# Kernel tuning notes

Hardware: AMD Instinct MI355X
Metric: run time of the kernel (lower is better)

The kernel has to match this reference:

```python
import jax, jax.numpy as jnp
import numpy as np

B, S, D, H = 4, 1024, 1024, 16
DEPTH = D // H


def setup_inputs() -> dict:
    key = jax.random.key(0)
    ks = jax.random.split(key, 12)
    scale = 1.0 / np.sqrt(D)
    return {
        "query": jax.random.normal(ks[0], (B, S, D), jnp.float32),
        "key_in": jax.random.normal(ks[1], (B, S, D), jnp.float32),
        "value": jax.random.normal(ks[2], (B, S, D), jnp.float32),
        "mask": jnp.zeros((B, 1, 1, S), jnp.float32),
        "wq": jax.random.normal(ks[3], (D, D), jnp.float32) * scale,
        "bq": jnp.zeros((D,), jnp.float32),
        "wk": jax.random.normal(ks[4], (D, D), jnp.float32) * scale,
        "bk": jnp.zeros((D,), jnp.float32),
        "wv": jax.random.normal(ks[5], (D, D), jnp.float32) * scale,
        "bv": jnp.zeros((D,), jnp.float32),
        "wo": jax.random.normal(ks[6], (D, D), jnp.float32) * scale,
        "bo": jnp.zeros((D,), jnp.float32),
    }


def _split_heads(x):
    b, s, _ = x.shape
    return x.reshape(b, s, H, DEPTH).transpose(0, 2, 1, 3)  # [B,H,S,depth]


def reference(query, key_in, value, mask, wq, bq, wk, bk, wv, bv, wo, bo):
    q = _split_heads(query @ wq + bq)
    k = _split_heads(key_in @ wk + bk)
    v = _split_heads(value @ wv + bv)
    # scaled dot-product attention, full O(S^2) scores as in the original
    scores = jnp.einsum("bhqd,bhkd->bhqk", q, k) / jnp.sqrt(jnp.float32(DEPTH))
    scores = scores + mask * (-1e9)
    attn = jax.nn.softmax(scores, axis=-1)
    ctx = jnp.einsum("bhqk,bhkd->bhqd", attn, v)
    concat = ctx.transpose(0, 2, 1, 3).reshape(query.shape[0], -1, D)
    return concat @ wo + bo
```

## Files before the change

### kernel.cpp

```cpp
#include <hip/hip_runtime.h>
#include <hip/hip_bf16.h>
#include <stdint.h>

#define B_ 4
#define S_ 1024
#define D_ 1024
#define H_ 16
#define DEPTH_ 64

typedef __attribute__((ext_vector_type(8))) short bf16x8;
typedef __attribute__((ext_vector_type(4))) float f32x4;
typedef unsigned short ubf16;

#define BAR() do { asm volatile("" ::: "memory"); __builtin_amdgcn_s_barrier(); asm volatile("" ::: "memory"); } while (0)

__device__ __forceinline__ ubf16 f2bf(float f) {
  union { float f; unsigned u; } v; v.f = f;
  unsigned r = v.u + 0x7fffu + ((v.u >> 16) & 1u);
  return (ubf16)(r >> 16);
}

__device__ __forceinline__ void async16(void* lds, const void* g) {
  __builtin_amdgcn_global_load_lds(
      (const __attribute__((address_space(1))) void*)g,
      (__attribute__((address_space(3))) void*)lds, 16, 0, 0);
}

struct Tp4 { const float* W[4]; ubf16* WT[4]; };
__global__ __launch_bounds__(256) void transpose4_bf16(Tp4 a) {
  __shared__ float tile[32][33];
  const float* W = a.W[blockIdx.z];
  ubf16* WT = a.WT[blockIdx.z];
  int n0 = blockIdx.x * 32, k0 = blockIdx.y * 32;
  int tx = threadIdx.x & 31, ty = threadIdx.x >> 5;
#pragma unroll
  for (int i = 0; i < 4; ++i)
    tile[ty + i * 8][tx] = W[(size_t)(k0 + ty + i * 8) * D_ + n0 + tx];
  __syncthreads();
#pragma unroll
  for (int i = 0; i < 4; ++i)
    WT[(size_t)(n0 + ty + i * 8) * D_ + k0 + tx] = f2bf(tile[tx][ty + i * 8]);
}

struct GemmUnitF {
  const float* A; const ubf16* BT; const float* bias; void* out; int mode;
};
struct GemmArgsF { GemmUnitF u[3]; };

__global__ __launch_bounds__(256) void gemm_qkv_fused(GemmArgsF args) {
  const GemmUnitF gu = args.u[blockIdx.z];
  const int orig = blockIdx.x + (blockIdx.y << 3);
  const int xcd = orig & 7, j = orig >> 3;
  const int bm0 = (xcd * 4 + (j & 3)) * 128;
  const int bn0 = (j >> 2) * 128;
  const int tid = threadIdx.x, wid = tid >> 6, lane = tid & 63;
  const int wr = wid >> 1, wc = wid & 1;
  const int l15 = lane & 15, l4 = lane >> 4;
  const int K = 1024;

  __shared__ __align__(16) ubf16 As[2][128 * 32];
  __shared__ __align__(16) ubf16 Bs[2][128 * 32];
  f32x4 acc[4][4] = {};

  int cc0, cc1;
  const float* aP0; const float* aP1;
  const ubf16* bP0; const ubf16* bP1;
  {
    cc0 = tid;           int r0 = cc0 >> 2, s0 = cc0 & 3, g0 = s0 ^ ((r0 >> 1) & 3);
    cc1 = 256 + tid;     int r1 = cc1 >> 2, s1 = cc1 & 3, g1 = s1 ^ ((r1 >> 1) & 3);
    aP0 = gu.A + (size_t)(bm0 + r0) * K + g0 * 8;
    aP1 = gu.A + (size_t)(bm0 + r1) * K + g1 * 8;
    bP0 = gu.BT + (size_t)(bn0 + r0) * K + g0 * 8;
    bP1 = gu.BT + (size_t)(bn0 + r1) * K + g1 * 8;
  }
  int aOff[4], bOff[4];
#pragma unroll
  for (int f = 0; f < 4; ++f) {
    int ra = wr * 64 + f * 16 + l15;
    aOff[f] = ra * 64 + (l4 ^ ((ra >> 1) & 3)) * 16;
    int rb = wc * 64 + f * 16 + l15;
    bOff[f] = rb * 64 + (l4 ^ ((rb >> 1) & 3)) * 16;
  }

  {
    f32x4 a00 = *(const f32x4*)aP0, a01 = *(const f32x4*)(aP0 + 4); aP0 += 32;
    f32x4 a10 = *(const f32x4*)aP1, a11 = *(const f32x4*)(aP1 + 4); aP1 += 32;
    async16((char*)&Bs[0][0] + wid * 1024, bP0); bP0 += 32;
    async16((char*)&Bs[0][0] + 4096 + wid * 1024, bP1); bP1 += 32;
    bf16x8 w0, w1;
#pragma unroll
    for (int q = 0; q < 4; ++q) {
      w0[q] = (short)f2bf(a00[q]); w0[4 + q] = (short)f2bf(a01[q]);
      w1[q] = (short)f2bf(a10[q]); w1[4 + q] = (short)f2bf(a11[q]);
    }
    *(bf16x8*)((char*)&As[0][0] + cc0 * 16) = w0;
    *(bf16x8*)((char*)&As[0][0] + cc1 * 16) = w1;
    asm volatile("s_waitcnt lgkmcnt(0)" ::: "memory");
  }

#pragma unroll 1
  for (int t = 0; t < 31; ++t) {
    const int cur = t & 1;
    f32x4 a00 = *(const f32x4*)aP0, a01 = *(const f32x4*)(aP0 + 4); aP0 += 32;
    f32x4 a10 = *(const f32x4*)aP1, a11 = *(const f32x4*)(aP1 + 4); aP1 += 32;
    async16((char*)&Bs[cur ^ 1][0] + wid * 1024, bP0); bP0 += 32;
    async16((char*)&Bs[cur ^ 1][0] + 4096 + wid * 1024, bP1); bP1 += 32;
    __builtin_amdgcn_sched_barrier(0);
    asm volatile("s_waitcnt vmcnt(4)" ::: "memory");
    __builtin_amdgcn_s_barrier();
    __builtin_amdgcn_sched_barrier(0);
    bf16x8 af[4], bfr[4];
#pragma unroll
    for (int mi = 0; mi < 4; ++mi)
      af[mi] = *(const bf16x8*)((const char*)&As[cur][0] + aOff[mi]);
#pragma unroll
    for (int ni = 0; ni < 4; ++ni)
      bfr[ni] = *(const bf16x8*)((const char*)&Bs[cur][0] + bOff[ni]);
#pragma unroll
    for (int mi = 0; mi < 4; ++mi)
#pragma unroll
      for (int ni = 0; ni < 4; ++ni)
        acc[mi][ni] = __builtin_amdgcn_mfma_f32_16x16x32_bf16(af[mi], bfr[ni], acc[mi][ni], 0, 0, 0);
    __builtin_amdgcn_sched_barrier(0);
    bf16x8 w0, w1;
#pragma unroll
    for (int q = 0; q < 4; ++q) {
      w0[q] = (short)f2bf(a00[q]); w0[4 + q] = (short)f2bf(a01[q]);
      w1[q] = (short)f2bf(a10[q]); w1[4 + q] = (short)f2bf(a11[q]);
    }
    *(bf16x8*)((char*)&As[cur ^ 1][0] + cc0 * 16) = w0;
    *(bf16x8*)((char*)&As[cur ^ 1][0] + cc1 * 16) = w1;
    asm volatile("s_waitcnt lgkmcnt(0)" ::: "memory");
    __builtin_amdgcn_s_barrier();
  }
  asm volatile("s_waitcnt vmcnt(0)" ::: "memory");
  __builtin_amdgcn_s_barrier();
  {
    bf16x8 af[4], bfr[4];
#pragma unroll
    for (int mi = 0; mi < 4; ++mi)
      af[mi] = *(const bf16x8*)((const char*)&As[1][0] + aOff[mi]);
#pragma unroll
    for (int ni = 0; ni < 4; ++ni)
      bfr[ni] = *(const bf16x8*)((const char*)&Bs[1][0] + bOff[ni]);
#pragma unroll
    for (int mi = 0; mi < 4; ++mi)
#pragma unroll
      for (int ni = 0; ni < 4; ++ni)
        acc[mi][ni] = __builtin_amdgcn_mfma_f32_16x16x32_bf16(af[mi], bfr[ni], acc[mi][ni], 0, 0, 0);
  }

  float bv[4];
#pragma unroll
  for (int ni = 0; ni < 4; ++ni) bv[ni] = gu.bias[bn0 + wc * 64 + ni * 16 + l15];
#pragma unroll
  for (int mi = 0; mi < 4; ++mi) {
#pragma unroll
    for (int ni = 0; ni < 4; ++ni) {
#pragma unroll
      for (int r = 0; r < 4; ++r) {
        int m = bm0 + wr * 64 + mi * 16 + l4 * 4 + r;
        int n = bn0 + wc * 64 + ni * 16 + l15;
        float v = acc[mi][ni][r] + bv[ni];
        if (gu.mode == 0) {
          ((ubf16*)gu.out)[(size_t)m * 1024 + n] = f2bf(v);
        } else {
          int b = m >> 10, s = m & 1023, h = n >> 6, d = n & 63;
          ((ubf16*)gu.out)[(((size_t)(b * H_ + h)) * DEPTH_ + d) * S_ + s] = f2bf(v);
        }
      }
    }
  }
}

struct GemmUnit {
  const ubf16* A; const ubf16* BT; const float* bias; void* out; int mode;
};
struct GemmArgs { GemmUnit u[3]; };

__global__ __launch_bounds__(256) void gemm_bt(GemmArgs args, int M, int N) {
  const GemmUnit gu = args.u[blockIdx.z];
  const int orig = blockIdx.x + (blockIdx.y << 3);
  const int xcd = orig & 7, j = orig >> 3;
  const int bm0 = (xcd * 4 + (j & 3)) * 128;
  const int bn0 = (j >> 2) * 128;
  const int tid = threadIdx.x, wid = tid >> 6, lane = tid & 63;
  const int wr = wid >> 1, wc = wid & 1;
  const int l15 = lane & 15, l4 = lane >> 4;
  const int K = 1024;

  __shared__ __align__(16) ubf16 As[2][128 * 32];
  __shared__ __align__(16) ubf16 Bs[2][128 * 32];
  f32x4 acc[4][4] = {};

  const ubf16* aCur[2]; const ubf16* bCur[2];
#pragma unroll
  for (int i = 0; i < 2; ++i) {
    int c = i * 256 + tid;
    int r = c >> 2, s = c & 3;
    int cg = s ^ ((r >> 1) & 3);
    aCur[i] = gu.A + (size_t)(bm0 + r) * K + cg * 8;
    bCur[i] = gu.BT + (size_t)(bn0 + r) * K + cg * 8;
  }
  auto stageAdv = [&](int bf) {
#pragma unroll
    for (int i = 0; i < 2; ++i) {
      async16((char*)&As[bf][0] + i * 4096 + wid * 1024, aCur[i]);
      async16((char*)&Bs[bf][0] + i * 4096 + wid * 1024, bCur[i]);
      aCur[i] += 32; bCur[i] += 32;
    }
  };
  int aOff[4], bOff[4];
#pragma unroll
  for (int f = 0; f < 4; ++f) {
    int ra = wr * 64 + f * 16 + l15;
    aOff[f] = ra * 64 + (l4 ^ ((ra >> 1) & 3)) * 16;
    int rb = wc * 64 + f * 16 + l15;
    bOff[f] = rb * 64 + (l4 ^ ((rb >> 1) & 3)) * 16;
  }

  stageAdv(0);
  for (int t = 0; t < 32; ++t) {
    const int cur = t & 1;
    if (t < 31) {
      stageAdv(cur ^ 1);
      asm volatile("s_waitcnt vmcnt(4)" ::: "memory");
    } else {
      asm volatile("s_waitcnt vmcnt(0)" ::: "memory");
    }
    BAR();
    bf16x8 af[4], bfr[4];
#pragma unroll
    for (int mi = 0; mi < 4; ++mi)
      af[mi] = *(const bf16x8*)((const char*)&As[cur][0] + aOff[mi]);
#pragma unroll
    for (int ni = 0; ni < 4; ++ni)
      bfr[ni] = *(const bf16x8*)((const char*)&Bs[cur][0] + bOff[ni]);
#pragma unroll
    for (int mi = 0; mi < 4; ++mi)
#pragma unroll
      for (int ni = 0; ni < 4; ++ni)
        acc[mi][ni] = __builtin_amdgcn_mfma_f32_16x16x32_bf16(af[mi], bfr[ni], acc[mi][ni], 0, 0, 0);
    BAR();
  }

  float bv[4];
#pragma unroll
  for (int ni = 0; ni < 4; ++ni) bv[ni] = gu.bias[bn0 + wc * 64 + ni * 16 + l15];
#pragma unroll
  for (int mi = 0; mi < 4; ++mi) {
#pragma unroll
    for (int ni = 0; ni < 4; ++ni) {
#pragma unroll
      for (int r = 0; r < 4; ++r) {
        int m = bm0 + wr * 64 + mi * 16 + l4 * 4 + r;
        int n = bn0 + wc * 64 + ni * 16 + l15;
        float v = acc[mi][ni][r] + bv[ni];
        if (gu.mode == 0) {
          ((ubf16*)gu.out)[(size_t)m * N + n] = f2bf(v);
        } else if (gu.mode == 1) {
          int b = m >> 10, s = m & 1023, h = n >> 6, d = n & 63;
          ((ubf16*)gu.out)[(((size_t)(b * H_ + h)) * DEPTH_ + d) * S_ + s] = f2bf(v);
        } else {
          ((float*)gu.out)[(size_t)m * N + n] = v;
        }
      }
    }
  }
}

__global__ __launch_bounds__(512) void attention_fwd(
    const ubf16* __restrict__ Q, const ubf16* __restrict__ Kg,
    const ubf16* __restrict__ VT, const float* __restrict__ mask,
    ubf16* __restrict__ ctx) {
  const int lid = blockIdx.y * 4 + blockIdx.x;
  const int t0 = (lid & 7) * 32 + (lid >> 3);
  const int qt = t0 & 3, bh = t0 >> 2;
  const int b = bh >> 4, h = bh & 15;
  const int tid = threadIdx.x, wid = tid >> 6, lane = tid & 63;
  const int l15 = lane & 15, l4 = lane >> 4;
  const int q0 = qt * 256 + wid * 32;

  __shared__ __align__(16) ubf16 Ks[2][4096];
  __shared__ __align__(16) ubf16 Vs[2][4096];
  __shared__ __align__(16) ubf16 Ps[8][32][72];

  const ubf16* kb = Kg + ((size_t)(b * S_)) * D_ + h * DEPTH_;
  const ubf16* vb = VT + ((size_t)bh) * DEPTH_ * S_;

  bf16x8 aq[2][2];
#pragma unroll
  for (int mi = 0; mi < 2; ++mi)
#pragma unroll
    for (int kk = 0; kk < 2; ++kk)
      aq[mi][kk] = *(const bf16x8*)&Q[((size_t)(b * S_ + q0 + mi * 16 + l15)) * D_ +
                                      h * DEPTH_ + kk * 32 + l4 * 8];

  bf16x8 ones;
#pragma unroll
  for (int j = 0; j < 8; ++j) ones[j] = (short)0x3F80;

  f32x4 cacc[2][4] = {};
  f32x4 csum[2] = {};

  const float* mrow = mask + b * S_;
  const float C1 = 0.125f * 1.44269504f;
  const float CM = -1.0e9f * 1.44269504f;

  auto stage = [&](int bf, int kt) {
    int r = tid >> 3, cg = (tid & 7) ^ (r & 7);
    async16((char*)&Ks[bf][0] + wid * 1024, kb + (size_t)(kt + r) * D_ + cg * 8);
    async16((char*)&Vs[bf][0] + wid * 1024, vb + (size_t)r * S_ + kt + cg * 8);
  };

  stage(0, 0);
  __syncthreads();

  for (int t = 0; t < 16; ++t) {
    const int cur = t & 1;
    const int kt = t * 64;
    if (t < 15) stage(cur ^ 1, kt + 64);

    bf16x8 kf[4][2];
#pragma unroll
    for (int nf = 0; nf < 4; ++nf)
#pragma unroll
      for (int kk = 0; kk < 2; ++kk) {
        int kr = nf * 16 + l15;
        int c16 = (kk * 4 + l4) ^ (kr & 7);
        kf[nf][kk] = *(const bf16x8*)((const char*)&Ks[cur][0] + kr * 128 + c16 * 16);
      }
    bf16x8 vf[4][2];
#pragma unroll
    for (int df = 0; df < 4; ++df)
#pragma unroll
      for (int kk = 0; kk < 2; ++kk) {
        int dr = df * 16 + l15;
        int c16 = (kk * 4 + l4) ^ (dr & 7);
        vf[df][kk] = *(const bf16x8*)((const char*)&Vs[cur][0] + dr * 128 + c16 * 16);
      }

    f32x4 sc[2][4];
#pragma unroll
    for (int mi = 0; mi < 2; ++mi)
#pragma unroll
      for (int nf = 0; nf < 4; ++nf) {
        f32x4 z = {0.f, 0.f, 0.f, 0.f};
        z = __builtin_amdgcn_mfma_f32_16x16x32_bf16(aq[mi][0], kf[nf][0], z, 0, 0, 0);
        z = __builtin_amdgcn_mfma_f32_16x16x32_bf16(aq[mi][1], kf[nf][1], z, 0, 0, 0);
        sc[mi][nf] = z;
      }

    float mvl[4];
#pragma unroll
    for (int nf = 0; nf < 4; ++nf) mvl[nf] = mrow[kt + nf * 16 + l15] * CM;

#pragma unroll
    for (int mi = 0; mi < 2; ++mi)
#pragma unroll
      for (int nf = 0; nf < 4; ++nf)
#pragma unroll
        for (int r = 0; r < 4; ++r) {
          float p = __builtin_amdgcn_exp2f(fmaf(sc[mi][nf][r], C1, mvl[nf]));
          Ps[wid][mi * 16 + l4 * 4 + r][nf * 16 + l15] = f2bf(p);
        }

    bf16x8 pf[2][2];
#pragma unroll
    for (int mi = 0; mi < 2; ++mi)
#pragma unroll
      for (int kk = 0; kk < 2; ++kk)
        pf[mi][kk] = *(const bf16x8*)&Ps[wid][mi * 16 + l15][kk * 32 + l4 * 8];

#pragma unroll
    for (int mi = 0; mi < 2; ++mi) {
#pragma unroll
      for (int df = 0; df < 4; ++df) {
        cacc[mi][df] = __builtin_amdgcn_mfma_f32_16x16x32_bf16(pf[mi][0], vf[df][0], cacc[mi][df], 0, 0, 0);
        cacc[mi][df] = __builtin_amdgcn_mfma_f32_16x16x32_bf16(pf[mi][1], vf[df][1], cacc[mi][df], 0, 0, 0);
      }
      csum[mi] = __builtin_amdgcn_mfma_f32_16x16x32_bf16(pf[mi][0], ones, csum[mi], 0, 0, 0);
      csum[mi] = __builtin_amdgcn_mfma_f32_16x16x32_bf16(pf[mi][1], ones, csum[mi], 0, 0, 0);
    }

    __syncthreads();
  }

#pragma unroll
  for (int mi = 0; mi < 2; ++mi) {
    float inv[4];
#pragma unroll
    for (int r = 0; r < 4; ++r) inv[r] = 1.0f / csum[mi][r];
#pragma unroll
    for (int df = 0; df < 4; ++df)
#pragma unroll
      for (int r = 0; r < 4; ++r) {
        int srow = q0 + mi * 16 + l4 * 4 + r;
        float v = cacc[mi][df][r] * inv[r];
        ctx[((size_t)(b * S_ + srow)) * D_ + h * DEPTH_ + df * 16 + l15] = f2bf(v);
      }
  }
}

extern "C" void kernel_launch(void* const* d_in, const int* in_sizes, int n_in,
                              void* d_out, int out_size, void* d_ws, size_t ws_size,
                              hipStream_t stream) {
  const float* query  = (const float*)d_in[0];
  const float* key_in = (const float*)d_in[1];
  const float* value  = (const float*)d_in[2];
  const float* mask   = (const float*)d_in[3];
  const float* wq = (const float*)d_in[4];
  const float* bq = (const float*)d_in[5];
  const float* wk = (const float*)d_in[6];
  const float* bk = (const float*)d_in[7];
  const float* wv = (const float*)d_in[8];
  const float* bv = (const float*)d_in[9];
  const float* wo = (const float*)d_in[10];
  const float* bo = (const float*)d_in[11];

  char* ws = (char*)d_ws;
  const size_t MB = 1024 * 1024;
  ubf16* WqT = (ubf16*)(ws + 24 * MB);
  ubf16* WkT = (ubf16*)(ws + 26 * MB);
  ubf16* WvT = (ubf16*)(ws + 28 * MB);
  ubf16* WoT = (ubf16*)(ws + 30 * MB);
  ubf16* Qb  = (ubf16*)(ws + 32 * MB);
  ubf16* Kb  = (ubf16*)(ws + 40 * MB);
  ubf16* VTb = (ubf16*)(ws + 48 * MB);
  ubf16* Ctx = (ubf16*)(ws + 56 * MB);

  Tp4 t4;
  t4.W[0] = wq; t4.WT[0] = WqT;
  t4.W[1] = wk; t4.WT[1] = WkT;
  t4.W[2] = wv; t4.WT[2] = WvT;
  t4.W[3] = wo; t4.WT[3] = WoT;
  transpose4_bf16<<<dim3(32, 32, 4), dim3(256), 0, stream>>>(t4);

  GemmArgsF g1;
  g1.u[0] = {query,  WqT, bq, (void*)Qb, 0};
  g1.u[1] = {key_in, WkT, bk, (void*)Kb, 0};
  g1.u[2] = {value,  WvT, bv, (void*)VTb, 1};
  gemm_qkv_fused<<<dim3(8, 32, 3), dim3(256), 0, stream>>>(g1);

  attention_fwd<<<dim3(4, 64), dim3(512), 0, stream>>>(Qb, Kb, VTb, mask, Ctx);

  GemmArgs g2;
  g2.u[0] = {Ctx, WoT, bo, d_out, 2};
  g2.u[1] = g2.u[0];
  g2.u[2] = g2.u[0];
  gemm_bt<<<dim3(8, 32, 1), dim3(256), 0, stream>>>(g2, 4096, 1024);
}
```

Before: 121.5 us.

## Enlarge QKV GEMM tile to 128x256 with 512 threads and XCD-aware 1D grid

The fused QKV projection GEMM now uses 128x256 output tiles computed by 8 waves (512 threads) instead of 128x128 tiles with 4 waves. Launch moves to a 1D grid of 384 workgroups remapped so consecutive tiles share an XCD. Each fp32 A row is now loaded and converted to bf16 once per 256 output columns rather than per 128, which halves redundant A reads and conversions. The trade-off is twice the LDS for B, half as many workgroups (384 on 256 CUs gives an uneven second wave), and more threads per block.

Result: slower. 135.7 us (+11.7%).

```diff
diff --git a/kernel.cpp b/kernel.cpp
--- a/kernel.cpp
+++ b/kernel.cpp
@@ -47,54 +47,53 @@
 };
 struct GemmArgsF { GemmUnitF u[3]; };
 
-__global__ __launch_bounds__(256) void gemm_qkv_fused(GemmArgsF args) {
-  const GemmUnitF gu = args.u[blockIdx.z];
-  const int orig = blockIdx.x + (blockIdx.y << 3);
-  const int xcd = orig & 7, j = orig >> 3;
-  const int bm0 = (xcd * 4 + (j & 3)) * 128;
-  const int bn0 = (j >> 2) * 128;
+__global__ __launch_bounds__(512) void gemm_qkv_fused(GemmArgsF args) {
+  const int lin = blockIdx.x;
+  const int wg = (lin & 7) * 48 + (lin >> 3);
+  const int z = wg >> 7, rr = wg & 127;
+  const GemmUnitF gu = args.u[z];
+  const int bm0 = (rr >> 2) * 128;
+  const int bn0 = (rr & 3) * 256;
   const int tid = threadIdx.x, wid = tid >> 6, lane = tid & 63;
-  const int wr = wid >> 1, wc = wid & 1;
+  const int wm = wid >> 2, wn = wid & 3;
   const int l15 = lane & 15, l4 = lane >> 4;
   const int K = 1024;
 
   __shared__ __align__(16) ubf16 As[2][128 * 32];
-  __shared__ __align__(16) ubf16 Bs[2][128 * 32];
+  __shared__ __align__(16) ubf16 Bs[2][256 * 32];
   f32x4 acc[4][4] = {};
 
-  int cc0, cc1;
-  const float* aP0; const float* aP1;
+  const float* aP0;
+  {
+    int r0 = tid >> 2, s0 = tid & 3, g0 = s0 ^ ((r0 >> 1) & 3);
+    aP0 = gu.A + (size_t)(bm0 + r0) * K + g0 * 8;
+  }
   const ubf16* bP0; const ubf16* bP1;
   {
-    cc0 = tid;           int r0 = cc0 >> 2, s0 = cc0 & 3, g0 = s0 ^ ((r0 >> 1) & 3);
-    cc1 = 256 + tid;     int r1 = cc1 >> 2, s1 = cc1 & 3, g1 = s1 ^ ((r1 >> 1) & 3);
-    aP0 = gu.A + (size_t)(bm0 + r0) * K + g0 * 8;
-    aP1 = gu.A + (size_t)(bm0 + r1) * K + g1 * 8;
+    int c0 = tid;        int r0 = c0 >> 2, s0 = c0 & 3, g0 = s0 ^ ((r0 >> 1) & 3);
+    int c1 = 512 + tid;  int r1 = c1 >> 2, s1 = c1 & 3, g1 = s1 ^ ((r1 >> 1) & 3);
     bP0 = gu.BT + (size_t)(bn0 + r0) * K + g0 * 8;
     bP1 = gu.BT + (size_t)(bn0 + r1) * K + g1 * 8;
   }
   int aOff[4], bOff[4];
 #pragma unroll
   for (int f = 0; f < 4; ++f) {
-    int ra = wr * 64 + f * 16 + l15;
+    int ra = wm * 64 + f * 16 + l15;
     aOff[f] = ra * 64 + (l4 ^ ((ra >> 1) & 3)) * 16;
-    int rb = wc * 64 + f * 16 + l15;
+    int rb = wn * 64 + f * 16 + l15;
     bOff[f] = rb * 64 + (l4 ^ ((rb >> 1) & 3)) * 16;
   }
 
   {
     f32x4 a00 = *(const f32x4*)aP0, a01 = *(const f32x4*)(aP0 + 4); aP0 += 32;
-    f32x4 a10 = *(const f32x4*)aP1, a11 = *(const f32x4*)(aP1 + 4); aP1 += 32;
     async16((char*)&Bs[0][0] + wid * 1024, bP0); bP0 += 32;
-    async16((char*)&Bs[0][0] + 4096 + wid * 1024, bP1); bP1 += 32;
-    bf16x8 w0, w1;
+    async16((char*)&Bs[0][0] + 8192 + wid * 1024, bP1); bP1 += 32;
+    bf16x8 w0;
 #pragma unroll
     for (int q = 0; q < 4; ++q) {
       w0[q] = (short)f2bf(a00[q]); w0[4 + q] = (short)f2bf(a01[q]);
-      w1[q] = (short)f2bf(a10[q]); w1[4 + q] = (short)f2bf(a11[q]);
-    }
-    *(bf16x8*)((char*)&As[0][0] + cc0 * 16) = w0;
-    *(bf16x8*)((char*)&As[0][0] + cc1 * 16) = w1;
+    }
+    *(bf16x8*)((char*)&As[0][0] + tid * 16) = w0;
     asm volatile("s_waitcnt lgkmcnt(0)" ::: "memory");
   }
 
@@ -102,9 +101,8 @@
   for (int t = 0; t < 31; ++t) {
     const int cur = t & 1;
     f32x4 a00 = *(const f32x4*)aP0, a01 = *(const f32x4*)(aP0 + 4); aP0 += 32;
-    f32x4 a10 = *(const f32x4*)aP1, a11 = *(const f32x4*)(aP1 + 4); aP1 += 32;
     async16((char*)&Bs[cur ^ 1][0] + wid * 1024, bP0); bP0 += 32;
-    async16((char*)&Bs[cur ^ 1][0] + 4096 + wid * 1024, bP1); bP1 += 32;
+    async16((char*)&Bs[cur ^ 1][0] + 8192 + wid * 1024, bP1); bP1 += 32;
     __builtin_amdgcn_sched_barrier(0);
     asm volatile("s_waitcnt vmcnt(4)" ::: "memory");
     __builtin_amdgcn_s_barrier();
@@ -122,14 +120,12 @@
       for (int ni = 0; ni < 4; ++ni)
         acc[mi][ni] = __builtin_amdgcn_mfma_f32_16x16x32_bf16(af[mi], bfr[ni], acc[mi][ni], 0, 0, 0);
     __builtin_amdgcn_sched_barrier(0);
-    bf16x8 w0, w1;
+    bf16x8 w0;
 #pragma unroll
     for (int q = 0; q < 4; ++q) {
       w0[q] = (short)f2bf(a00[q]); w0[4 + q] = (short)f2bf(a01[q]);
-      w1[q] = (short)f2bf(a10[q]); w1[4 + q] = (short)f2bf(a11[q]);
-    }
-    *(bf16x8*)((char*)&As[cur ^ 1][0] + cc0 * 16) = w0;
-    *(bf16x8*)((char*)&As[cur ^ 1][0] + cc1 * 16) = w1;
+    }
+    *(bf16x8*)((char*)&As[cur ^ 1][0] + tid * 16) = w0;
     asm volatile("s_waitcnt lgkmcnt(0)" ::: "memory");
     __builtin_amdgcn_s_barrier();
   }
@@ -152,15 +148,15 @@
 
   float bv[4];
 #pragma unroll
-  for (int ni = 0; ni < 4; ++ni) bv[ni] = gu.bias[bn0 + wc * 64 + ni * 16 + l15];
+  for (int ni = 0; ni < 4; ++ni) bv[ni] = gu.bias[bn0 + wn * 64 + ni * 16 + l15];
 #pragma unroll
   for (int mi = 0; mi < 4; ++mi) {
 #pragma unroll
     for (int ni = 0; ni < 4; ++ni) {
 #pragma unroll
       for (int r = 0; r < 4; ++r) {
-        int m = bm0 + wr * 64 + mi * 16 + l4 * 4 + r;
-        int n = bn0 + wc * 64 + ni * 16 + l15;
+        int m = bm0 + wm * 64 + mi * 16 + l4 * 4 + r;
+        int n = bn0 + wn * 64 + ni * 16 + l15;
         float v = acc[mi][ni][r] + bv[ni];
         if (gu.mode == 0) {
           ((ubf16*)gu.out)[(size_t)m * 1024 + n] = f2bf(v);
@@ -440,7 +436,7 @@
   g1.u[0] = {query,  WqT, bq, (void*)Qb, 0};
   g1.u[1] = {key_in, WkT, bk, (void*)Kb, 0};
   g1.u[2] = {value,  WvT, bv, (void*)VTb, 1};
-  gemm_qkv_fused<<<dim3(8, 32, 3), dim3(256), 0, stream>>>(g1);
+  gemm_qkv_fused<<<dim3(384), dim3(512), 0, stream>>>(g1);
 
   attention_fwd<<<dim3(4, 64), dim3(512), 0, stream>>>(Qb, Kb, VTb, mask, Ctx);
 
```
